# Performance work log

Hardware: AMD Instinct MI355X
Metric: run time of the kernel (lower is better)

## Reference

```python
import jax, jax.numpy as jnp
import numpy as np

B, L, D = 4, 4096, 256
INIT_ALPHA = -2.0
INV_TEMP = 1.0 / 0.1


def setup_inputs() -> dict:
    key = jax.random.key(0)
    k1, k2, k3, k4 = jax.random.split(key, 4)
    latents = jax.random.normal(k1, (B, L, D), dtype=jnp.float32)
    current_coords = jax.random.normal(k2, (B, L, 2), dtype=jnp.float32)
    # Linear(D, D, bias=False) weights (torch stores [out, in]; y = x @ W.T)
    lim = 1.0 / np.sqrt(D)
    Wq = jax.random.uniform(k3, (D, D), minval=-lim, maxval=lim, dtype=jnp.float32)
    Wk = jax.random.uniform(k4, (D, D), minval=-lim, maxval=lim, dtype=jnp.float32)
    alpha_raw = jnp.asarray(INIT_ALPHA, dtype=jnp.float32)
    return {"latents": latents, "current_coords": current_coords,
            "Wq": Wq, "Wk": Wk, "alpha_raw": alpha_raw, "layer_idx": 3}


def _l2norm(x, eps=1e-12):
    # F.normalize(dim=-1): x / max(||x||, eps)
    n = jnp.sqrt(jnp.sum(x * x, axis=-1, keepdims=True))
    return x / jnp.maximum(n, eps)


def reference(latents, current_coords, Wq, Wk, alpha_raw, layer_idx):
    # pred_idx selection (share_weights=True): 0 if layer_idx==0 else 1;
    # layer_idx=3 -> params given are for pred_idx=1.
    q = _l2norm(jnp.einsum('bld,ed->ble', latents, Wq))  # [B,L,D]
    k = _l2norm(jnp.einsum('bld,ed->ble', latents, Wk))  # [B,L,D]
    scores = jnp.einsum('bld,bmd->blm', q, k) * INV_TEMP  # [B,L,L]
    scores = jnp.clip(scores, -50.0, 50.0)
    W = jax.nn.softmax(scores, axis=-1)                   # [B,L,L]
    alpha = jax.nn.sigmoid(alpha_raw)
    # M = alpha*W + (1-alpha)*I; M @ coords == alpha*(W@coords) + (1-alpha)*coords
    new_coords = alpha * jnp.einsum('blm,bmc->blc', W, current_coords) \
                 + (1.0 - alpha) * current_coords
    displacement = new_coords - current_coords
    return (new_coords, displacement)
```

## Files before the change

### kernel.cpp

```cpp
#include <hip/hip_runtime.h>
#include <hip/hip_bf16.h>

#define BB 4
#define LL 4096
#define DD 256
#define MM (BB * LL)
#define NSPLIT 8
#define BM 256
#define NQB (LL / BM)
#define KPS (LL / NSPLIT)
#define KT 64
#define NKT (KPS / KT)

typedef short short8 __attribute__((ext_vector_type(8)));
typedef float floatx4 __attribute__((ext_vector_type(4)));

#define SCALE_LOG2E 14.426950408889634f

__device__ __forceinline__ unsigned short f2bf(float f) {
    __hip_bfloat16 h = __float2bfloat16(f);
    union { __hip_bfloat16 h; unsigned short s; } c; c.h = h; return c.s;
}

__device__ __forceinline__ float fast_exp2(float x) {
#if __has_builtin(__builtin_amdgcn_exp2f)
    return __builtin_amdgcn_exp2f(x);
#else
    return exp2f(x);
#endif
}

__device__ __forceinline__ void stage16(const char* g, char* l, int lane) {
#if __has_builtin(__builtin_amdgcn_global_load_lds)
    __builtin_amdgcn_global_load_lds(
        (const __attribute__((address_space(1))) void*)(g + lane * 16),
        (__attribute__((address_space(3))) void*)l, 16, 0, 0);
#else
    *(short8*)(l + lane * 16) = *(const short8*)(g + lane * 16);
#endif
}

__global__ __launch_bounds__(256) void cvt_swz_kernel(
    const float* __restrict__ srcq, const float* __restrict__ srck,
    unsigned short* __restrict__ dstq, unsigned short* __restrict__ dstk)
{
    const int which = blockIdx.x >> 5;
    const float* src = which ? srck : srcq;
    unsigned short* dst = which ? dstk : dstq;
    const int t = (blockIdx.x & 31) * 256 + threadIdx.x;
    const int r = t >> 5, c = t & 31;
    const float4 v0 = ((const float4*)src)[t * 2];
    const float4 v1 = ((const float4*)src)[t * 2 + 1];
    short8 o;
    o[0] = (short)f2bf(v0.x); o[1] = (short)f2bf(v0.y);
    o[2] = (short)f2bf(v0.z); o[3] = (short)f2bf(v0.w);
    o[4] = (short)f2bf(v1.x); o[5] = (short)f2bf(v1.y);
    o[6] = (short)f2bf(v1.z); o[7] = (short)f2bf(v1.w);
    const int cs = c ^ (r & 7);
    *(short8*)(dst + (size_t)r * DD + cs * 8) = o;
}

__global__ __launch_bounds__(256) void proj_norm_kernel(
    const float* __restrict__ latents,
    const __hip_bfloat16* __restrict__ Wq,
    const __hip_bfloat16* __restrict__ Wk,
    __hip_bfloat16* __restrict__ qn,
    __hip_bfloat16* __restrict__ kn)
{
    __shared__ char lds[65536];

    const int tid  = threadIdx.x;
    const int wave = tid >> 6;
    const int lane = tid & 63;
    const int n15  = lane & 15;
    const int quad = lane >> 4;
    const int sw   = n15 & 7;

    const int pass  = blockIdx.x & 1;
    const int rbase = (blockIdx.x >> 1) * 64;
    const int m0    = rbase + wave * 16;
    const int r160  = rbase >> 4;

    short8 afrag[8];
    const float* Abase = latents + (size_t)(m0 + n15) * DD + quad * 8;
#pragma unroll
    for (int kk = 0; kk < 8; ++kk) {
        const float4 v0 = *(const float4*)(Abase + kk * 32);
        const float4 v1 = *(const float4*)(Abase + kk * 32 + 4);
        short8 f;
        f[0] = (short)f2bf(v0.x); f[1] = (short)f2bf(v0.y);
        f[2] = (short)f2bf(v0.z); f[3] = (short)f2bf(v0.w);
        f[4] = (short)f2bf(v1.x); f[5] = (short)f2bf(v1.y);
        f[6] = (short)f2bf(v1.z); f[7] = (short)f2bf(v1.w);
        afrag[kk] = f;
    }

    const char* W = (const char*)(pass ? Wk : Wq);

    floatx4 acc[16];
#pragma unroll
    for (int ct = 0; ct < 16; ++ct) acc[ct] = (floatx4){0.f, 0.f, 0.f, 0.f};

    {
        const char* src = W + wave * 8192;
        char* dst = lds + wave * 8192;
#pragma unroll
        for (int j = 0; j < 8; ++j) stage16(src + j * 1024, dst + j * 1024, lane);
    }

    for (int round = 0; round < 4; ++round) {
        __syncthreads();
        if (round + 1 < 4) {
            const char* src = W + (size_t)(round + 1) * 32768 + wave * 8192;
            char* dst = lds + ((round + 1) & 1) * 32768 + wave * 8192;
#pragma unroll
            for (int j = 0; j < 8; ++j) stage16(src + j * 1024, dst + j * 1024, lane);
        }
        const char* buf = lds + (round & 1) * 32768;
#pragma unroll
        for (int jt = 0; jt < 4; ++jt) {
            const int ct = round * 4 + jt;
            const char* lbase = buf + (jt * 16 + n15) * 512;
            floatx4 a = acc[ct];
#pragma unroll
            for (int kk = 0; kk < 8; ++kk) {
                const int chunk = (4 * kk + quad) ^ sw;
                short8 bfr = *(const short8*)(lbase + chunk * 16);
                a = __builtin_amdgcn_mfma_f32_16x16x32_bf16(afrag[kk], bfr, a, 0, 0, 0);
            }
            acc[ct] = a;
        }
    }

    float ss[4] = {0.f, 0.f, 0.f, 0.f};
#pragma unroll
    for (int ct = 0; ct < 16; ++ct)
#pragma unroll
        for (int r = 0; r < 4; ++r) ss[r] += acc[ct][r] * acc[ct][r];
#pragma unroll
    for (int r = 0; r < 4; ++r) {
        ss[r] += __shfl_xor(ss[r], 1, 64);
        ss[r] += __shfl_xor(ss[r], 2, 64);
        ss[r] += __shfl_xor(ss[r], 4, 64);
        ss[r] += __shfl_xor(ss[r], 8, 64);
    }
    float sc[4];
#pragma unroll
    for (int r = 0; r < 4; ++r) {
        sc[r] = 1.f / fmaxf(sqrtf(ss[r]), 1e-12f);
        if (pass == 0) sc[r] *= SCALE_LOG2E;
    }

    unsigned short* tb = (unsigned short*)lds;
#pragma unroll
    for (int h = 0; h < 2; ++h) {
        __syncthreads();
#pragma unroll
        for (int cth = 0; cth < 8; ++cth) {
            const int ct = h * 8 + cth;
            const int col = cth * 16 + n15;
#pragma unroll
            for (int r = 0; r < 4; ++r) {
                const int rl = wave * 16 + quad * 4 + r;
                tb[rl * 136 + col] = f2bf(acc[ct][r] * sc[r]);
            }
        }
        __syncthreads();
        if (pass == 0) {
#pragma unroll
            for (int j = 0; j < 4; ++j) {
                const int g = tid + j * 256;
                const int n15r = g & 15, q2 = (g >> 4) & 3, kkh = (g >> 6) & 3, r16l = (g >> 8) & 3;
                const int rl = r16l * 16 + n15r;
                short8 v = *(const short8*)(tb + rl * 136 + kkh * 32 + q2 * 8);
                const size_t chunk = (((size_t)(r160 + r16l) * 8 + (h * 4 + kkh)) * 4 + q2) * 16 + n15r;
                *(short8*)((char*)qn + chunk * 16) = v;
            }
        } else {
#pragma unroll
            for (int j = 0; j < 4; ++j) {
                const int g = tid + j * 256;
                const int csl = g & 15, rl = g >> 4;
                const int row = rbase + rl;
                const int ci = csl ^ (row & 7);
                short8 v = *(const short8*)(tb + rl * 136 + ci * 8);
                *(short8*)((char*)kn + (size_t)row * 512 + (h * 16 + csl) * 16) = v;
            }
        }
    }
}

__global__ __launch_bounds__(256, 2) void attn_kernel(
    const __hip_bfloat16* __restrict__ qn,
    const __hip_bfloat16* __restrict__ kn,
    const float* __restrict__ coords,
    float* __restrict__ partials)
{
    __shared__ char lds[2 * 32768];

    const int tid  = threadIdx.x;
    const int wave = tid >> 6;
    const int lane = tid & 63;
    const int n15  = lane & 15;
    const int quad = lane >> 4;
    const int sw   = n15 & 7;

    int bs = (blockIdx.x & 7) * 64 + (blockIdx.x >> 3);
    const int qb    = bs % NQB;    bs /= NQB;
    const int split = bs % NSPLIT; bs /= NSPLIT;
    const int b     = bs;

    const int mw = b * LL + qb * BM + wave * 64;

    const int key_base = b * LL + split * KPS;
    const char* ksrc = (const char*)kn + (size_t)key_base * 512;

    {
        const char* src = ksrc + wave * 8192;
        char* dst = lds + wave * 8192;
#pragma unroll
        for (int j = 0; j < 8; ++j) stage16(src + j * 1024, dst + j * 1024, lane);
    }

    short8 aq[4][8];
    const int t16 = mw >> 4;
#pragma unroll
    for (int rt = 0; rt < 4; ++rt)
#pragma unroll
        for (int kk = 0; kk < 8; ++kk) {
            const size_t chunk = (((size_t)(t16 + rt) * 8 + kk) * 4 + quad) * 16 + n15;
            aq[rt][kk] = *(const short8*)((const char*)qn + chunk * 16);
        }

    float s0[4][4], s1[4][4], s2[4][4];
#pragma unroll
    for (int rt = 0; rt < 4; ++rt)
#pragma unroll
        for (int r = 0; r < 4; ++r) { s0[rt][r] = 0.f; s1[rt][r] = 0.f; s2[rt][r] = 0.f; }

    for (int kt = 0; kt < NKT; ++kt) {
        __syncthreads();
        if (kt + 1 < NKT) {
            const char* src = ksrc + (size_t)(kt + 1) * KT * 512 + wave * 8192;
            char* dst = lds + ((kt + 1) & 1) * 32768 + wave * 8192;
#pragma unroll
            for (int j = 0; j < 8; ++j) stage16(src + j * 1024, dst + j * 1024, lane);
        }
        const char* buf = lds + (kt & 1) * 32768;

#pragma unroll
        for (int ct = 0; ct < 4; ++ct) {
            const int kidx = key_base + kt * KT + ct * 16 + n15;
            const float2 cc = *(const float2*)(coords + (size_t)kidx * 2);

            floatx4 acc[4];
#pragma unroll
            for (int rt = 0; rt < 4; ++rt) acc[rt] = (floatx4){0.f, 0.f, 0.f, 0.f};
            const char* lbase = buf + (ct * 16 + n15) * 512;
#pragma unroll
            for (int kk = 0; kk < 8; ++kk) {
                const int chunk = (4 * kk + quad) ^ sw;
                const short8 bfr = *(const short8*)(lbase + chunk * 16);
#pragma unroll
                for (int rt = 0; rt < 4; ++rt)
                    acc[rt] = __builtin_amdgcn_mfma_f32_16x16x32_bf16(aq[rt][kk], bfr, acc[rt], 0, 0, 0);
            }
#pragma unroll
            for (int rt = 0; rt < 4; ++rt)
#pragma unroll
                for (int r = 0; r < 4; ++r) {
                    const float e = fast_exp2(acc[rt][r]);
                    s0[rt][r] += e;
                    s1[rt][r] = fmaf(cc.x, e, s1[rt][r]);
                    s2[rt][r] = fmaf(cc.y, e, s2[rt][r]);
                }
        }
    }

#pragma unroll
    for (int rt = 0; rt < 4; ++rt)
#pragma unroll
        for (int r = 0; r < 4; ++r)
#pragma unroll
            for (int mask = 1; mask <= 8; mask <<= 1) {
                s0[rt][r] += __shfl_xor(s0[rt][r], mask, 64);
                s1[rt][r] += __shfl_xor(s1[rt][r], mask, 64);
                s2[rt][r] += __shfl_xor(s2[rt][r], mask, 64);
            }

    if (n15 == 0) {
#pragma unroll
        for (int rt = 0; rt < 4; ++rt)
#pragma unroll
            for (int r = 0; r < 4; ++r) {
                const int m = mw + rt * 16 + quad * 4 + r;
                float* p = partials + ((size_t)split * MM + m) * 4;
                p[0] = s0[rt][r];
                p[1] = s1[rt][r];
                p[2] = s2[rt][r];
            }
    }
}

__global__ __launch_bounds__(256) void finish_kernel(
    const float* __restrict__ partials,
    const float* __restrict__ coords,
    const float* __restrict__ alpha_raw,
    float* __restrict__ out)
{
    const int m = blockIdx.x * 256 + threadIdx.x;

    const float alpha = 1.f / (1.f + __expf(-alpha_raw[0]));

    float s0 = 0.f, s1 = 0.f, s2 = 0.f;
#pragma unroll
    for (int s = 0; s < NSPLIT; ++s) {
        const float4 v = *(const float4*)(partials + ((size_t)s * MM + m) * 4);
        s0 += v.x; s1 += v.y; s2 += v.z;
    }

    const float cx = coords[m * 2];
    const float cy = coords[m * 2 + 1];
    const float inv = 1.f / s0;
    const float nx = alpha * (s1 * inv) + (1.f - alpha) * cx;
    const float ny = alpha * (s2 * inv) + (1.f - alpha) * cy;

    out[m * 2]     = nx;
    out[m * 2 + 1] = ny;
    out[2 * MM + m * 2]     = nx - cx;
    out[2 * MM + m * 2 + 1] = ny - cy;
}

extern "C" void kernel_launch(void* const* d_in, const int* in_sizes, int n_in,
                              void* d_out, int out_size, void* d_ws, size_t ws_size,
                              hipStream_t stream) {
    const float* latents   = (const float*)d_in[0];
    const float* coords    = (const float*)d_in[1];
    const float* Wq        = (const float*)d_in[2];
    const float* Wk        = (const float*)d_in[3];
    const float* alpha_raw = (const float*)d_in[4];

    char* ws = (char*)d_ws;
    __hip_bfloat16* qn   = (__hip_bfloat16*)ws;
    __hip_bfloat16* kn   = (__hip_bfloat16*)(ws + (size_t)8 * 1024 * 1024);
    __hip_bfloat16* wq_b = (__hip_bfloat16*)(ws + (size_t)16 * 1024 * 1024);
    __hip_bfloat16* wk_b = (__hip_bfloat16*)(ws + (size_t)16 * 1024 * 1024 + 131072);
    float* partials      = (float*)(ws + (size_t)16 * 1024 * 1024 + 262144);

    float* out = (float*)d_out;

    cvt_swz_kernel<<<64, 256, 0, stream>>>(Wq, Wk, (unsigned short*)wq_b, (unsigned short*)wk_b);
    proj_norm_kernel<<<512, 256, 0, stream>>>(latents, wq_b, wk_b, qn, kn);
    attn_kernel<<<BB * NQB * NSPLIT, 256, 0, stream>>>(qn, kn, coords, partials);
    finish_kernel<<<MM / 256, 256, 0, stream>>>(partials, coords, alpha_raw, out);
}
```

Baseline: 126.4 us.

## Prefetch two key tiles ahead with explicit vmcnt waits and stage coords in LDS

The attention kernel now issues loads for the first two key tiles after the Q fragments and replaces __syncthreads with explicit s_waitcnt vmcnt counts plus raw barriers. This keeps one tile in flight while the other is computed, and the next refill is issued after a second barrier. Coordinates for the split are staged once into LDS rather than read from global memory on every tile. MFMA sections in both kernels are wrapped in s_setprio, and an asm register pin keeps the Q fragments in registers. The hand-counted vmcnt values depend on the exact load count per tile and are fragile if the compiler reorders or splits loads.

```diff
diff --git a/kernel.cpp b/kernel.cpp
--- a/kernel.cpp
+++ b/kernel.cpp
@@ -28,6 +28,10 @@
 #else
     return exp2f(x);
 #endif
+}
+
+__device__ __forceinline__ void pinv(short8& v) {
+    asm volatile("" : "+v"(v));
 }
 
 __device__ __forceinline__ void stage16(const char* g, char* l, int lane) {
@@ -122,12 +126,14 @@
             const int ct = round * 4 + jt;
             const char* lbase = buf + (jt * 16 + n15) * 512;
             floatx4 a = acc[ct];
+            __builtin_amdgcn_s_setprio(1);
 #pragma unroll
             for (int kk = 0; kk < 8; ++kk) {
                 const int chunk = (4 * kk + quad) ^ sw;
                 short8 bfr = *(const short8*)(lbase + chunk * 16);
                 a = __builtin_amdgcn_mfma_f32_16x16x32_bf16(afrag[kk], bfr, a, 0, 0, 0);
             }
+            __builtin_amdgcn_s_setprio(0);
             acc[ct] = a;
         }
     }
@@ -196,7 +202,8 @@
     const float* __restrict__ coords,
     float* __restrict__ partials)
 {
-    __shared__ char lds[2 * 32768];
+    __shared__ char lds[2 * 32768 + 4096];
+    char* clds = lds + 2 * 32768;
 
     const int tid  = threadIdx.x;
     const int wave = tid >> 6;
@@ -215,12 +222,9 @@
     const int key_base = b * LL + split * KPS;
     const char* ksrc = (const char*)kn + (size_t)key_base * 512;
 
-    {
-        const char* src = ksrc + wave * 8192;
-        char* dst = lds + wave * 8192;
-#pragma unroll
-        for (int j = 0; j < 8; ++j) stage16(src + j * 1024, dst + j * 1024, lane);
-    }
+    stage16((const char*)coords + (size_t)key_base * 8 + wave * 1024,
+            clds + wave * 1024, lane);
+    asm volatile("" ::: "memory");
 
     short8 aq[4][8];
     const int t16 = mw >> 4;
@@ -231,6 +235,20 @@
             const size_t chunk = (((size_t)(t16 + rt) * 8 + kk) * 4 + quad) * 16 + n15;
             aq[rt][kk] = *(const short8*)((const char*)qn + chunk * 16);
         }
+#pragma unroll
+    for (int rt = 0; rt < 4; ++rt)
+#pragma unroll
+        for (int kk = 0; kk < 8; ++kk) pinv(aq[rt][kk]);
+    asm volatile("" ::: "memory");
+
+#pragma unroll
+    for (int t = 0; t < 2; ++t) {
+        const char* src = ksrc + (size_t)t * KT * 512 + wave * 8192;
+        char* dst = lds + t * 32768 + wave * 8192;
+#pragma unroll
+        for (int j = 0; j < 8; ++j) stage16(src + j * 1024, dst + j * 1024, lane);
+        asm volatile("" ::: "memory");
+    }
 
     float s0[4][4], s1[4][4], s2[4][4];
 #pragma unroll
@@ -238,25 +256,24 @@
 #pragma unroll
         for (int r = 0; r < 4; ++r) { s0[rt][r] = 0.f; s1[rt][r] = 0.f; s2[rt][r] = 0.f; }
 
+#pragma unroll
     for (int kt = 0; kt < NKT; ++kt) {
-        __syncthreads();
-        if (kt + 1 < NKT) {
-            const char* src = ksrc + (size_t)(kt + 1) * KT * 512 + wave * 8192;
-            char* dst = lds + ((kt + 1) & 1) * 32768 + wave * 8192;
-#pragma unroll
-            for (int j = 0; j < 8; ++j) stage16(src + j * 1024, dst + j * 1024, lane);
-        }
+        if (kt == NKT - 1) asm volatile("s_waitcnt vmcnt(0)" ::: "memory");
+        else               asm volatile("s_waitcnt vmcnt(8)" ::: "memory");
+        __builtin_amdgcn_s_barrier();
+
         const char* buf = lds + (kt & 1) * 32768;
 
 #pragma unroll
         for (int ct = 0; ct < 4; ++ct) {
-            const int kidx = key_base + kt * KT + ct * 16 + n15;
-            const float2 cc = *(const float2*)(coords + (size_t)kidx * 2);
+            const float2 cc = *(const float2*)(clds + (kt * KT + ct * 16 + n15) * 8);
 
             floatx4 acc[4];
 #pragma unroll
             for (int rt = 0; rt < 4; ++rt) acc[rt] = (floatx4){0.f, 0.f, 0.f, 0.f};
             const char* lbase = buf + (ct * 16 + n15) * 512;
+
+            __builtin_amdgcn_s_setprio(1);
 #pragma unroll
             for (int kk = 0; kk < 8; ++kk) {
                 const int chunk = (4 * kk + quad) ^ sw;
@@ -265,6 +282,8 @@
                 for (int rt = 0; rt < 4; ++rt)
                     acc[rt] = __builtin_amdgcn_mfma_f32_16x16x32_bf16(aq[rt][kk], bfr, acc[rt], 0, 0, 0);
             }
+            __builtin_amdgcn_s_setprio(0);
+
 #pragma unroll
             for (int rt = 0; rt < 4; ++rt)
 #pragma unroll
@@ -274,6 +293,15 @@
                     s1[rt][r] = fmaf(cc.x, e, s1[rt][r]);
                     s2[rt][r] = fmaf(cc.y, e, s2[rt][r]);
                 }
+        }
+
+        if (kt + 2 < NKT) {
+            __builtin_amdgcn_s_barrier();
+            const char* src = ksrc + (size_t)(kt + 2) * KT * 512 + wave * 8192;
+            char* dst = lds + (kt & 1) * 32768 + wave * 8192;
+#pragma unroll
+            for (int j = 0; j < 8; ++j) stage16(src + j * 1024, dst + j * 1024, lane);
+            asm volatile("" ::: "memory");
         }
     }
 
```

Measured after the change: 124.6 us. No clear change (-1.4%).

## Store K and weights in MFMA fragment-major layout and prioritize MFMA waves

Applied to the files above, without the earlier changes.

Weights and normalized keys are now written in fragment-major order, the same layout already used for queries. LDS B-operand reads therefore become contiguous lane*16 loads with no XOR swizzle. The change also wraps the MFMA loops in s_setprio, regroups proj_norm blocks so eight consecutive blocks share a pass, drops the occupancy hint of 2 on attn_kernel, and pins the Q fragments in registers with an empty asm. The goal is cheaper LDS address math and conflict-free reads, at the cost of possible register pressure or changed occupancy in the attention kernel.

```diff
diff --git a/kernel.cpp b/kernel.cpp
--- a/kernel.cpp
+++ b/kernel.cpp
@@ -17,6 +17,7 @@
 
 #define SCALE_LOG2E 14.426950408889634f
 
+
 __device__ __forceinline__ unsigned short f2bf(float f) {
     __hip_bfloat16 h = __float2bfloat16(f);
     union { __hip_bfloat16 h; unsigned short s; } c; c.h = h; return c.s;
@@ -28,6 +29,10 @@
 #else
     return exp2f(x);
 #endif
+}
+
+__device__ __forceinline__ void pinv(short8& v) {
+    asm volatile("" : "+v"(v));
 }
 
 __device__ __forceinline__ void stage16(const char* g, char* l, int lane) {
@@ -40,7 +45,7 @@
 #endif
 }
 
-__global__ __launch_bounds__(256) void cvt_swz_kernel(
+__global__ __launch_bounds__(256) void cvt_fm_kernel(
     const float* __restrict__ srcq, const float* __restrict__ srck,
     unsigned short* __restrict__ dstq, unsigned short* __restrict__ dstk)
 {
@@ -56,8 +61,8 @@
     o[2] = (short)f2bf(v0.z); o[3] = (short)f2bf(v0.w);
     o[4] = (short)f2bf(v1.x); o[5] = (short)f2bf(v1.y);
     o[6] = (short)f2bf(v1.z); o[7] = (short)f2bf(v1.w);
-    const int cs = c ^ (r & 7);
-    *(short8*)(dst + (size_t)r * DD + cs * 8) = o;
+    const int chunk = (r >> 4) * 512 + c * 16 + (r & 15);
+    *(short8*)(dst + (size_t)chunk * 8) = o;
 }
 
 __global__ __launch_bounds__(256) void proj_norm_kernel(
@@ -74,10 +79,10 @@
     const int lane = tid & 63;
     const int n15  = lane & 15;
     const int quad = lane >> 4;
-    const int sw   = n15 & 7;
-
-    const int pass  = blockIdx.x & 1;
-    const int rbase = (blockIdx.x >> 1) * 64;
+
+    const int pass  = (blockIdx.x >> 3) & 1;
+    const int pidx  = (blockIdx.x & 7) | ((blockIdx.x >> 4) << 3);
+    const int rbase = pidx * 64;
     const int m0    = rbase + wave * 16;
     const int r160  = rbase >> 4;
 
@@ -120,14 +125,15 @@
 #pragma unroll
         for (int jt = 0; jt < 4; ++jt) {
             const int ct = round * 4 + jt;
-            const char* lbase = buf + (jt * 16 + n15) * 512;
+            const char* lbase = buf + jt * 8192 + lane * 16;
             floatx4 a = acc[ct];
+            __builtin_amdgcn_s_setprio(1);
 #pragma unroll
             for (int kk = 0; kk < 8; ++kk) {
-                const int chunk = (4 * kk + quad) ^ sw;
-                short8 bfr = *(const short8*)(lbase + chunk * 16);
+                short8 bfr = *(const short8*)(lbase + kk * 1024);
                 a = __builtin_amdgcn_mfma_f32_16x16x32_bf16(afrag[kk], bfr, a, 0, 0, 0);
             }
+            __builtin_amdgcn_s_setprio(0);
             acc[ct] = a;
         }
     }
@@ -151,6 +157,7 @@
         if (pass == 0) sc[r] *= SCALE_LOG2E;
     }
 
+    __hip_bfloat16* dstp = pass ? kn : qn;
     unsigned short* tb = (unsigned short*)lds;
 #pragma unroll
     for (int h = 0; h < 2; ++h) {
@@ -166,31 +173,19 @@
             }
         }
         __syncthreads();
-        if (pass == 0) {
-#pragma unroll
-            for (int j = 0; j < 4; ++j) {
-                const int g = tid + j * 256;
-                const int n15r = g & 15, q2 = (g >> 4) & 3, kkh = (g >> 6) & 3, r16l = (g >> 8) & 3;
-                const int rl = r16l * 16 + n15r;
-                short8 v = *(const short8*)(tb + rl * 136 + kkh * 32 + q2 * 8);
-                const size_t chunk = (((size_t)(r160 + r16l) * 8 + (h * 4 + kkh)) * 4 + q2) * 16 + n15r;
-                *(short8*)((char*)qn + chunk * 16) = v;
-            }
-        } else {
-#pragma unroll
-            for (int j = 0; j < 4; ++j) {
-                const int g = tid + j * 256;
-                const int csl = g & 15, rl = g >> 4;
-                const int row = rbase + rl;
-                const int ci = csl ^ (row & 7);
-                short8 v = *(const short8*)(tb + rl * 136 + ci * 8);
-                *(short8*)((char*)kn + (size_t)row * 512 + (h * 16 + csl) * 16) = v;
-            }
-        }
-    }
-}
-
-__global__ __launch_bounds__(256, 2) void attn_kernel(
+#pragma unroll
+        for (int j = 0; j < 4; ++j) {
+            const int g = tid + j * 256;
+            const int n15r = g & 15, q2 = (g >> 4) & 3, kkh = (g >> 6) & 3, r16l = (g >> 8) & 3;
+            const int rl = r16l * 16 + n15r;
+            short8 v = *(const short8*)(tb + rl * 136 + kkh * 32 + q2 * 8);
+            const size_t chunk = (((size_t)(r160 + r16l) * 8 + (h * 4 + kkh)) * 4 + q2) * 16 + n15r;
+            *(short8*)((char*)dstp + chunk * 16) = v;
+        }
+    }
+}
+
+__global__ __launch_bounds__(256) void attn_kernel(
     const __hip_bfloat16* __restrict__ qn,
     const __hip_bfloat16* __restrict__ kn,
     const float* __restrict__ coords,
@@ -203,7 +198,6 @@
     const int lane = tid & 63;
     const int n15  = lane & 15;
     const int quad = lane >> 4;
-    const int sw   = n15 & 7;
 
     int bs = (blockIdx.x & 7) * 64 + (blockIdx.x >> 3);
     const int qb    = bs % NQB;    bs /= NQB;
@@ -231,6 +225,10 @@
             const size_t chunk = (((size_t)(t16 + rt) * 8 + kk) * 4 + quad) * 16 + n15;
             aq[rt][kk] = *(const short8*)((const char*)qn + chunk * 16);
         }
+#pragma unroll
+    for (int rt = 0; rt < 4; ++rt)
+#pragma unroll
+        for (int kk = 0; kk < 8; ++kk) pinv(aq[rt][kk]);
 
     float s0[4][4], s1[4][4], s2[4][4];
 #pragma unroll
@@ -256,15 +254,18 @@
             floatx4 acc[4];
 #pragma unroll
             for (int rt = 0; rt < 4; ++rt) acc[rt] = (floatx4){0.f, 0.f, 0.f, 0.f};
-            const char* lbase = buf + (ct * 16 + n15) * 512;
+            const char* lbase = buf + ct * 8192 + lane * 16;
+
+            __builtin_amdgcn_s_setprio(1);
 #pragma unroll
             for (int kk = 0; kk < 8; ++kk) {
-                const int chunk = (4 * kk + quad) ^ sw;
-                const short8 bfr = *(const short8*)(lbase + chunk * 16);
+                const short8 bfr = *(const short8*)(lbase + kk * 1024);
 #pragma unroll
                 for (int rt = 0; rt < 4; ++rt)
                     acc[rt] = __builtin_amdgcn_mfma_f32_16x16x32_bf16(aq[rt][kk], bfr, acc[rt], 0, 0, 0);
             }
+            __builtin_amdgcn_s_setprio(0);
+
 #pragma unroll
             for (int rt = 0; rt < 4; ++rt)
 #pragma unroll
@@ -349,7 +350,7 @@
 
     float* out = (float*)d_out;
 
-    cvt_swz_kernel<<<64, 256, 0, stream>>>(Wq, Wk, (unsigned short*)wq_b, (unsigned short*)wk_b);
+    cvt_fm_kernel<<<64, 256, 0, stream>>>(Wq, Wk, (unsigned short*)wq_b, (unsigned short*)wk_b);
     proj_norm_kernel<<<512, 256, 0, stream>>>(latents, wq_b, wk_b, qn, kn);
     attn_kernel<<<BB * NQB * NSPLIT, 256, 0, stream>>>(qn, kn, coords, partials);
     finish_kernel<<<MM / 256, 256, 0, stream>>>(partials, coords, alpha_raw, out);
```

New measurement: 136.2 us. 1.08x slower.
